# Kernel optimization log

Hardware: AMD Instinct MI355X
Metric: run time of the kernel (lower is better)

Reference implementation:

```python
import jax, jax.numpy as jnp
import numpy as np
from jax.ops import segment_sum

NUM_EMBEDDINGS = 512
EMBEDDING_DIM = 64
COMMITMENT_COST = 0.25
DECAY = 0.99
EPSILON = 1e-05


def setup_inputs() -> dict:
    key = jax.random.key(0)
    k1, k2, k3 = jax.random.split(key, 3)
    B, C, T = 32, EMBEDDING_DIM, 4096
    z = jax.random.normal(k1, (B, C, T), dtype=jnp.float32)
    embedding = jax.random.normal(k2, (NUM_EMBEDDINGS, EMBEDDING_DIM), dtype=jnp.float32)
    cluster_size = jnp.zeros((NUM_EMBEDDINGS,), dtype=jnp.float32)
    embed_avg = jax.random.normal(k3, (NUM_EMBEDDINGS, EMBEDDING_DIM), dtype=jnp.float32)
    return {"z": z, "embedding": embedding, "cluster_size": cluster_size, "embed_avg": embed_avg}


def reference(z, embedding, cluster_size, embed_avg):
    B, C, T = z.shape
    K = embedding.shape[0]
    # flatten: (B, C, T) -> (B*T, C), matching reshape(B,C,-1).permute(0,2,1).reshape(-1,C)
    z_flat = jnp.transpose(z, (0, 2, 1)).reshape(-1, C)  # [N, C]
    N = z_flat.shape[0]

    # squared-euclidean nearest-code search (argmin of cdist == argmin of sq dist)
    d2 = (jnp.sum(z_flat * z_flat, axis=1, keepdims=True)
          - 2.0 * (z_flat @ embedding.T)
          + jnp.sum(embedding * embedding, axis=1)[None, :])  # [N, K]
    indices = jnp.argmin(d2, axis=1)  # [N] int

    # quantize: gather instead of one-hot matmul (same math)
    quantized_flat = embedding[indices]  # [N, C]
    quantized = jnp.transpose(quantized_flat.reshape(B, T, C), (0, 2, 1))  # [B, C, T]

    # EMA codebook update (training branch)
    n = segment_sum(jnp.ones((N,), dtype=z.dtype), indices, num_segments=K)  # [K]
    new_cluster_size = cluster_size * DECAY + (1.0 - DECAY) * n
    embed_sum = segment_sum(z_flat, indices, num_segments=K)  # [K, C]
    new_embed_avg = embed_avg * DECAY + (1.0 - DECAY) * embed_sum
    n_tot = jnp.sum(new_cluster_size)
    cs_smoothed = (new_cluster_size + EPSILON) / (n_tot + K * EPSILON) * n_tot
    new_embedding = new_embed_avg / cs_smoothed[:, None]

    # commitment loss against detached quantized
    commitment_loss = jnp.mean((z - jax.lax.stop_gradient(quantized)) ** 2)
    vq_loss = COMMITMENT_COST * commitment_loss

    # straight-through estimator
    quantized_st = z + jax.lax.stop_gradient(quantized - z)

    # perplexity over code usage (zero-count codes contribute ~0, as in torch unique version)
    probs = n / N
    perplexity = jnp.exp(-jnp.sum(probs * jnp.log(probs + 1e-10)))

    return (quantized_st, indices, vq_loss, perplexity,
            new_embedding, new_cluster_size, new_embed_avg)
```

## Files before the change

kernel.cpp:

```cpp
#include <hip/hip_runtime.h>
#include <math.h>

#define KB_NUM 512
#define DIMC 64
#define BSZ 32
#define TLEN 4096
#define NTOK (BSZ * TLEN)
#define DECAY_F 0.99f
#define EPS_F 1e-5f
#define K2_SPAN 512

#define Q_OFF    ((size_t)0)
#define IDX_OFF  ((size_t)BSZ * DIMC * TLEN)
#define LOSS_OFF (IDX_OFF + (size_t)NTOK)
#define PLEX_OFF (LOSS_OFF + 1)
#define NEMB_OFF (PLEX_OFF + 1)
#define NCS_OFF  (NEMB_OFF + (size_t)KB_NUM * DIMC)
#define NEA_OFF  (NCS_OFF + (size_t)KB_NUM)

typedef _Float16 f16x8 __attribute__((ext_vector_type(8)));
typedef float    f32x4 __attribute__((ext_vector_type(4)));

__global__ __launch_bounds__(64) void vq_prep_e(
    const float* __restrict__ emb,
    _Float16* __restrict__ eh,
    _Float16* __restrict__ el,
    float* __restrict__ enorm)
{
    const int k = blockIdx.x;
    const int c = threadIdx.x;
    float v = emb[(size_t)k * DIMC + c];
    _Float16 h = (_Float16)v;
    eh[(size_t)k * DIMC + c] = h;
    el[(size_t)k * DIMC + c] = (_Float16)(v - (float)h);
    float s = v * v;
    #pragma unroll
    for (int off = 32; off > 0; off >>= 1)
        s += __shfl_down(s, off, 64);
    if (c == 0) enorm[k] = 0.5f * s;
}

__global__ __launch_bounds__(256, 2) void vq_main_kernel(
    const float* __restrict__ z,
    const float* __restrict__ emb,
    const _Float16* __restrict__ eh,
    const _Float16* __restrict__ el,
    const float* __restrict__ enorm,
    float* __restrict__ out,
    float* __restrict__ lossAcc)
{
    __shared__ float zs[256 * 65];

    const int tid = threadIdx.x;
    const int w   = tid >> 6;
    const int ln  = tid & 63;
    const int bk  = blockIdx.x;
    const int b   = bk >> 4;
    const int t0  = (bk & 15) << 8;

    const float* zg = z + (size_t)b * (DIMC * TLEN) + t0;

    #pragma unroll 8
    for (int c = 0; c < DIMC; ++c)
        zs[tid * 65 + c] = zg[(size_t)c * TLEN + tid];
    __syncthreads();

    f16x8 zhf[4][2], zlf[4][2];
    #pragma unroll
    for (int tt = 0; tt < 4; ++tt) {
        #pragma unroll
        for (int ks = 0; ks < 2; ++ks) {
            const float* zrow = &zs[(w * 64 + tt * 16 + (ln & 15)) * 65
                                    + ks * 32 + ((ln >> 4) << 3)];
            #pragma unroll
            for (int j = 0; j < 8; ++j) {
                float v = zrow[j];
                _Float16 h = (_Float16)v;
                zhf[tt][ks][j] = h;
                zlf[tt][ks][j] = (_Float16)(v - (float)h);
            }
        }
    }

    float bv[4] = {3.4e38f, 3.4e38f, 3.4e38f, 3.4e38f};
    int   bi[4] = {0, 0, 0, 0};

    #pragma unroll 1
    for (int chunk = 0; chunk < 8; ++chunk) {
        f32x4 acc[4][4];
        #pragma unroll
        for (int ct = 0; ct < 4; ++ct)
            #pragma unroll
            for (int tt = 0; tt < 4; ++tt)
                acc[ct][tt] = (f32x4){0.f, 0.f, 0.f, 0.f};

        #pragma unroll
        for (int ct = 0; ct < 4; ++ct) {
            const int crow = chunk * 64 + ct * 16 + (ln & 15);
            f16x8 ah[2], al[2];
            #pragma unroll
            for (int ks = 0; ks < 2; ++ks) {
                const size_t aoff = (size_t)crow * DIMC + ks * 32 + ((ln >> 4) << 3);
                ah[ks] = *(const f16x8*)(eh + aoff);
                al[ks] = *(const f16x8*)(el + aoff);
            }
            #pragma unroll
            for (int ks = 0; ks < 2; ++ks) {
                #pragma unroll
                for (int tt = 0; tt < 4; ++tt)
                    acc[ct][tt] = __builtin_amdgcn_mfma_f32_16x16x32_f16(
                        ah[ks], zhf[tt][ks], acc[ct][tt], 0, 0, 0);
                #pragma unroll
                for (int tt = 0; tt < 4; ++tt)
                    acc[ct][tt] = __builtin_amdgcn_mfma_f32_16x16x32_f16(
                        ah[ks], zlf[tt][ks], acc[ct][tt], 0, 0, 0);
                #pragma unroll
                for (int tt = 0; tt < 4; ++tt)
                    acc[ct][tt] = __builtin_amdgcn_mfma_f32_16x16x32_f16(
                        al[ks], zhf[tt][ks], acc[ct][tt], 0, 0, 0);
                #pragma unroll
                for (int tt = 0; tt < 4; ++tt)
                    acc[ct][tt] = __builtin_amdgcn_mfma_f32_16x16x32_f16(
                        al[ks], zlf[tt][ks], acc[ct][tt], 0, 0, 0);
            }
        }

        #pragma unroll
        for (int ct = 0; ct < 4; ++ct) {
            const int cb = chunk * 64 + ct * 16 + ((ln >> 4) << 2);
            float4 en = *(const float4*)(enorm + cb);
            const float e0 = en.x, e1 = en.y, e2 = en.z, e3 = en.w;
            #pragma unroll
            for (int tt = 0; tt < 4; ++tt) {
                float s0 = e0 - acc[ct][tt][0];
                float s1 = e1 - acc[ct][tt][1];
                float s2 = e2 - acc[ct][tt][2];
                float s3 = e3 - acc[ct][tt][3];
                if (s0 < bv[tt]) { bv[tt] = s0; bi[tt] = cb; }
                if (s1 < bv[tt]) { bv[tt] = s1; bi[tt] = cb + 1; }
                if (s2 < bv[tt]) { bv[tt] = s2; bi[tt] = cb + 2; }
                if (s3 < bv[tt]) { bv[tt] = s3; bi[tt] = cb + 3; }
            }
        }
    }

    #pragma unroll
    for (int mask = 16; mask <= 32; mask <<= 1) {
        #pragma unroll
        for (int tt = 0; tt < 4; ++tt) {
            float ov = __shfl_xor(bv[tt], mask, 64);
            int   oi = __shfl_xor(bi[tt], mask, 64);
            if (ov < bv[tt] || (ov == bv[tt] && oi < bi[tt])) {
                bv[tt] = ov; bi[tt] = oi;
            }
        }
    }

    const int g = ln >> 4;
    const int idxv = (g == 0) ? bi[0] : (g == 1) ? bi[1] : (g == 2) ? bi[2] : bi[3];
    const int tok = w * 64 + ln;

    out[IDX_OFF + (size_t)b * TLEN + t0 + tok] = (float)idxv;

    const float* er   = emb + (size_t)idxv * DIMC;
    const float* zrow = &zs[tok * 65];
    float* qo = out + (size_t)b * (DIMC * TLEN) + t0 + tok;

    float lsum = 0.f;
    #pragma unroll
    for (int c4 = 0; c4 < DIMC / 4; ++c4) {
        float4 ev = *(const float4*)(er + c4 * 4);
        float z0 = zrow[c4 * 4 + 0], z1 = zrow[c4 * 4 + 1];
        float z2 = zrow[c4 * 4 + 2], z3 = zrow[c4 * 4 + 3];
        float d0 = ev.x - z0, d1 = ev.y - z1, d2 = ev.z - z2, d3 = ev.w - z3;
        qo[(size_t)(c4 * 4 + 0) * TLEN] = z0 + d0;
        qo[(size_t)(c4 * 4 + 1) * TLEN] = z1 + d1;
        qo[(size_t)(c4 * 4 + 2) * TLEN] = z2 + d2;
        qo[(size_t)(c4 * 4 + 3) * TLEN] = z3 + d3;
        lsum = fmaf(d0, d0, lsum); lsum = fmaf(d1, d1, lsum);
        lsum = fmaf(d2, d2, lsum); lsum = fmaf(d3, d3, lsum);
    }

    #pragma unroll
    for (int off = 32; off > 0; off >>= 1)
        lsum += __shfl_down(lsum, off, 64);
    if (ln == 0) atomicAdd(lossAcc, lsum);
}

__global__ __launch_bounds__(256, 1) void vq_bin_kernel(
    const float* __restrict__ z,
    const float* __restrict__ out,
    float* __restrict__ cnt,
    float* __restrict__ esum,
    int R)
{
    __shared__ float acc[KB_NUM][DIMC + 1];
    __shared__ float scnt[KB_NUM];

    const int tid = threadIdx.x;
    for (int j = tid; j < KB_NUM * (DIMC + 1); j += 256) ((float*)acc)[j] = 0.f;
    for (int j = tid; j < KB_NUM; j += 256) scnt[j] = 0.f;
    __syncthreads();

    const int gt0 = blockIdx.x * K2_SPAN;
    #pragma unroll
    for (int it = 0; it < K2_SPAN / 256; ++it) {
        const int gt = gt0 + it * 256 + tid;
        const int b  = gt >> 12;
        const int t  = gt & (TLEN - 1);
        const int idx = (int)out[IDX_OFF + gt];
        atomicAdd(&scnt[idx], 1.0f);
        const float* zp = z + (size_t)b * (DIMC * TLEN) + t;
        #pragma unroll 4
        for (int c = 0; c < DIMC; ++c) {
            float zv = zp[(size_t)c * TLEN];
            atomicAdd(&acc[idx][c], zv);
        }
    }
    __syncthreads();

    const int r = (int)((unsigned)blockIdx.x % (unsigned)R);
    for (int j = tid; j < KB_NUM * DIMC; j += 256) {
        const int k = j >> 6, c = j & 63;
        float v = acc[k][c];
        if (v != 0.f) atomicAdd(esum + (size_t)r * (KB_NUM * DIMC) + j, v);
    }
    for (int j = tid; j < KB_NUM; j += 256) {
        float v = scnt[j];
        if (v != 0.f) atomicAdd(cnt + (size_t)r * KB_NUM + j, v);
    }
}

__global__ __launch_bounds__(512) void vq_stats_kernel(
    const float* __restrict__ cluster_size,
    const float* __restrict__ cnt,
    const float* __restrict__ lossAcc,
    float* __restrict__ out,
    float* __restrict__ ntotp,
    int R)
{
    const int k = threadIdx.x;

    float n = 0.f;
    #pragma unroll 4
    for (int r = 0; r < R; ++r) n += cnt[(size_t)r * KB_NUM + k];

    float ncs = cluster_size[k] * DECAY_F + (1.0f - DECAY_F) * n;
    out[NCS_OFF + k] = ncs;

    __shared__ float red[KB_NUM];

    red[k] = ncs;
    __syncthreads();
    for (int s = KB_NUM / 2; s > 0; s >>= 1) {
        if (k < s) red[k] += red[k + s];
        __syncthreads();
    }
    if (k == 0) ntotp[0] = red[0];
    __syncthreads();

    float p = n * (1.0f / (float)NTOK);
    red[k] = p * logf(p + 1e-10f);
    __syncthreads();
    for (int s = KB_NUM / 2; s > 0; s >>= 1) {
        if (k < s) red[k] += red[k + s];
        __syncthreads();
    }
    if (k == 0) {
        out[PLEX_OFF] = expf(-red[0]);
        out[LOSS_OFF] = 0.25f * lossAcc[0] * (1.0f / (float)(BSZ * DIMC * TLEN));
    }
}

__global__ __launch_bounds__(64) void vq_embed_kernel(
    const float* __restrict__ embed_avg,
    const float* __restrict__ esum,
    const float* __restrict__ ntotp,
    float* __restrict__ out,
    int R)
{
    const int k = blockIdx.x;
    const int c = threadIdx.x;

    float es = 0.f;
    #pragma unroll 4
    for (int r = 0; r < R; ++r)
        es += esum[((size_t)r * KB_NUM + k) * DIMC + c];

    float nea = embed_avg[(size_t)k * DIMC + c] * DECAY_F + (1.0f - DECAY_F) * es;
    out[NEA_OFF + (size_t)k * DIMC + c] = nea;

    float ncs  = out[NCS_OFF + k];
    float ntot = ntotp[0];
    float denom = (ncs + EPS_F) / (ntot + (float)KB_NUM * EPS_F) * ntot;
    out[NEMB_OFF + (size_t)k * DIMC + c] = nea / denom;
}

extern "C" void kernel_launch(void* const* d_in, const int* in_sizes, int n_in,
                              void* d_out, int out_size, void* d_ws, size_t ws_size,
                              hipStream_t stream)
{
    const float* z            = (const float*)d_in[0];
    const float* emb          = (const float*)d_in[1];
    const float* cluster_size = (const float*)d_in[2];
    const float* embed_avg    = (const float*)d_in[3];
    float* out = (float*)d_out;

    char* ws = (char*)d_ws;
    float*     lossAcc = (float*)ws;
    float*     ntotp   = (float*)(ws + 64);
    float*     enorm   = (float*)(ws + 256);
    _Float16*  eh      = (_Float16*)(ws + 4096);
    _Float16*  el      = (_Float16*)(ws + 4096 + 65536);
    const size_t CNT_OFF = 4096 + 131072;
    const size_t perR = (size_t)(KB_NUM + KB_NUM * DIMC) * sizeof(float);

    int R = 1;
    if (ws_size > CNT_OFF + perR)
        R = (int)((ws_size - CNT_OFF) / perR);
    if (R < 1) R = 1;
    if (R > 16) R = 16;

    float* cnt  = (float*)(ws + CNT_OFF);
    float* esum = cnt + (size_t)R * KB_NUM;

    hipMemsetAsync(ws, 0, 4096, stream);
    hipMemsetAsync(ws + CNT_OFF, 0, (size_t)R * perR, stream);

    vq_prep_e<<<dim3(KB_NUM), dim3(DIMC), 0, stream>>>(emb, eh, el, enorm);

    vq_main_kernel<<<dim3(NTOK / 256), dim3(256), 0, stream>>>(
        z, emb, eh, el, enorm, out, lossAcc);

    vq_bin_kernel<<<dim3(NTOK / K2_SPAN), dim3(256), 0, stream>>>(z, out, cnt, esum, R);

    vq_stats_kernel<<<dim3(1), dim3(512), 0, stream>>>(
        cluster_size, cnt, lossAcc, out, ntotp, R);

    vq_embed_kernel<<<dim3(KB_NUM), dim3(DIMC), 0, stream>>>(
        embed_avg, esum, ntotp, out, R);
}
```

Baseline: 153.7 us.

## Halve tokens per block in VQ search kernel and raise occupancy

```diff
diff --git a/kernel.cpp b/kernel.cpp
--- a/kernel.cpp
+++ b/kernel.cpp
@@ -9,6 +9,7 @@
 #define DECAY_F 0.99f
 #define EPS_F 1e-5f
 #define K2_SPAN 512
+#define MTOK 128
 
 #define Q_OFF    ((size_t)0)
 #define IDX_OFF  ((size_t)BSZ * DIMC * TLEN)
@@ -40,7 +41,7 @@
     if (c == 0) enorm[k] = 0.5f * s;
 }
 
-__global__ __launch_bounds__(256, 2) void vq_main_kernel(
+__global__ __launch_bounds__(256, 4) void vq_main_kernel(
     const float* __restrict__ z,
     const float* __restrict__ emb,
     const _Float16* __restrict__ eh,
@@ -49,28 +50,32 @@
     float* __restrict__ out,
     float* __restrict__ lossAcc)
 {
-    __shared__ float zs[256 * 65];
+    __shared__ float zs[MTOK * 65];
 
     const int tid = threadIdx.x;
     const int w   = tid >> 6;
     const int ln  = tid & 63;
     const int bk  = blockIdx.x;
-    const int b   = bk >> 4;
-    const int t0  = (bk & 15) << 8;
+    const int b   = bk >> 5;
+    const int t0  = (bk & 31) << 7;
 
     const float* zg = z + (size_t)b * (DIMC * TLEN) + t0;
 
-    #pragma unroll 8
-    for (int c = 0; c < DIMC; ++c)
-        zs[tid * 65 + c] = zg[(size_t)c * TLEN + tid];
-    __syncthreads();
-
-    f16x8 zhf[4][2], zlf[4][2];
-    #pragma unroll
-    for (int tt = 0; tt < 4; ++tt) {
+    {
+        const int tok   = tid & (MTOK - 1);
+        const int chalf = (tid >> 7) * 32;
+        #pragma unroll 8
+        for (int j = 0; j < 32; ++j)
+            zs[tok * 65 + chalf + j] = zg[(size_t)(chalf + j) * TLEN + tok];
+    }
+    __syncthreads();
+
+    f16x8 zhf[2][2], zlf[2][2];
+    #pragma unroll
+    for (int tt = 0; tt < 2; ++tt) {
         #pragma unroll
         for (int ks = 0; ks < 2; ++ks) {
-            const float* zrow = &zs[(w * 64 + tt * 16 + (ln & 15)) * 65
+            const float* zrow = &zs[(w * 32 + tt * 16 + (ln & 15)) * 65
                                     + ks * 32 + ((ln >> 4) << 3)];
             #pragma unroll
             for (int j = 0; j < 8; ++j) {
@@ -82,16 +87,16 @@
         }
     }
 
-    float bv[4] = {3.4e38f, 3.4e38f, 3.4e38f, 3.4e38f};
-    int   bi[4] = {0, 0, 0, 0};
+    float bv[2] = {3.4e38f, 3.4e38f};
+    int   bi[2] = {0, 0};
 
     #pragma unroll 1
     for (int chunk = 0; chunk < 8; ++chunk) {
-        f32x4 acc[4][4];
+        f32x4 acc[4][2];
         #pragma unroll
         for (int ct = 0; ct < 4; ++ct)
             #pragma unroll
-            for (int tt = 0; tt < 4; ++tt)
+            for (int tt = 0; tt < 2; ++tt)
                 acc[ct][tt] = (f32x4){0.f, 0.f, 0.f, 0.f};
 
         #pragma unroll
@@ -107,19 +112,19 @@
             #pragma unroll
             for (int ks = 0; ks < 2; ++ks) {
                 #pragma unroll
-                for (int tt = 0; tt < 4; ++tt)
+                for (int tt = 0; tt < 2; ++tt)
                     acc[ct][tt] = __builtin_amdgcn_mfma_f32_16x16x32_f16(
                         ah[ks], zhf[tt][ks], acc[ct][tt], 0, 0, 0);
                 #pragma unroll
-                for (int tt = 0; tt < 4; ++tt)
+                for (int tt = 0; tt < 2; ++tt)
                     acc[ct][tt] = __builtin_amdgcn_mfma_f32_16x16x32_f16(
                         ah[ks], zlf[tt][ks], acc[ct][tt], 0, 0, 0);
                 #pragma unroll
-                for (int tt = 0; tt < 4; ++tt)
+                for (int tt = 0; tt < 2; ++tt)
                     acc[ct][tt] = __builtin_amdgcn_mfma_f32_16x16x32_f16(
                         al[ks], zhf[tt][ks], acc[ct][tt], 0, 0, 0);
                 #pragma unroll
-                for (int tt = 0; tt < 4; ++tt)
+                for (int tt = 0; tt < 2; ++tt)
                     acc[ct][tt] = __builtin_amdgcn_mfma_f32_16x16x32_f16(
                         al[ks], zlf[tt][ks], acc[ct][tt], 0, 0, 0);
             }
@@ -131,7 +136,7 @@
             float4 en = *(const float4*)(enorm + cb);
             const float e0 = en.x, e1 = en.y, e2 = en.z, e3 = en.w;
             #pragma unroll
-            for (int tt = 0; tt < 4; ++tt) {
+            for (int tt = 0; tt < 2; ++tt) {
                 float s0 = e0 - acc[ct][tt][0];
                 float s1 = e1 - acc[ct][tt][1];
                 float s2 = e2 - acc[ct][tt][2];
@@ -147,7 +152,7 @@
     #pragma unroll
     for (int mask = 16; mask <= 32; mask <<= 1) {
         #pragma unroll
-        for (int tt = 0; tt < 4; ++tt) {
+        for (int tt = 0; tt < 2; ++tt) {
             float ov = __shfl_xor(bv[tt], mask, 64);
             int   oi = __shfl_xor(bi[tt], mask, 64);
             if (ov < bv[tt] || (ov == bv[tt] && oi < bi[tt])) {
@@ -156,19 +161,21 @@
         }
     }
 
-    const int g = ln >> 4;
-    const int idxv = (g == 0) ? bi[0] : (g == 1) ? bi[1] : (g == 2) ? bi[2] : bi[3];
-    const int tok = w * 64 + ln;
-
-    out[IDX_OFF + (size_t)b * TLEN + t0 + tok] = (float)idxv;
-
-    const float* er   = emb + (size_t)idxv * DIMC;
-    const float* zrow = &zs[tok * 65];
-    float* qo = out + (size_t)b * (DIMC * TLEN) + t0 + tok;
+    const int tte   = ln >> 5;
+    const int idxv  = tte ? bi[1] : bi[0];
+    const int tok   = w * 32 + tte * 16 + (ln & 15);
+    const int chalf = ((ln >> 4) & 1) * 32;
+
+    if (((ln >> 4) & 1) == 0)
+        out[IDX_OFF + (size_t)b * TLEN + t0 + tok] = (float)idxv;
+
+    const float* er   = emb + (size_t)idxv * DIMC + chalf;
+    const float* zrow = &zs[tok * 65 + chalf];
+    float* qo = out + (size_t)b * (DIMC * TLEN) + t0 + tok + (size_t)chalf * TLEN;
 
     float lsum = 0.f;
     #pragma unroll
-    for (int c4 = 0; c4 < DIMC / 4; ++c4) {
+    for (int c4 = 0; c4 < 8; ++c4) {
         float4 ev = *(const float4*)(er + c4 * 4);
         float z0 = zrow[c4 * 4 + 0], z1 = zrow[c4 * 4 + 1];
         float z2 = zrow[c4 * 4 + 2], z3 = zrow[c4 * 4 + 3];
@@ -324,12 +331,11 @@
     float* cnt  = (float*)(ws + CNT_OFF);
     float* esum = cnt + (size_t)R * KB_NUM;
 
-    hipMemsetAsync(ws, 0, 4096, stream);
-    hipMemsetAsync(ws + CNT_OFF, 0, (size_t)R * perR, stream);
+    hipMemsetAsync(ws, 0, CNT_OFF + (size_t)R * perR, stream);
 
     vq_prep_e<<<dim3(KB_NUM), dim3(DIMC), 0, stream>>>(emb, eh, el, enorm);
 
-    vq_main_kernel<<<dim3(NTOK / 256), dim3(256), 0, stream>>>(
+    vq_main_kernel<<<dim3(NTOK / MTOK), dim3(256), 0, stream>>>(
         z, emb, eh, el, enorm, out, lossAcc);
 
     vq_bin_kernel<<<dim3(NTOK / K2_SPAN), dim3(256), 0, stream>>>(z, out, cnt, esum, R);
```

After: 199.4 us. 1.3x slower.

## Pre-swizzle codebook into MFMA fragment layout and vectorize binning kernel

Applied to the files above, without the earlier changes.

```diff
diff --git a/kernel.cpp b/kernel.cpp
--- a/kernel.cpp
+++ b/kernel.cpp
@@ -8,7 +8,6 @@
 #define NTOK (BSZ * TLEN)
 #define DECAY_F 0.99f
 #define EPS_F 1e-5f
-#define K2_SPAN 512
 
 #define Q_OFF    ((size_t)0)
 #define IDX_OFF  ((size_t)BSZ * DIMC * TLEN)
@@ -23,16 +22,22 @@
 
 __global__ __launch_bounds__(64) void vq_prep_e(
     const float* __restrict__ emb,
-    _Float16* __restrict__ eh,
-    _Float16* __restrict__ el,
+    _Float16* __restrict__ efrag,
     float* __restrict__ enorm)
 {
     const int k = blockIdx.x;
     const int c = threadIdx.x;
     float v = emb[(size_t)k * DIMC + c];
     _Float16 h = (_Float16)v;
-    eh[(size_t)k * DIMC + c] = h;
-    el[(size_t)k * DIMC + c] = (_Float16)(v - (float)h);
+    _Float16 l = (_Float16)(v - (float)h);
+
+    const int kgrp = k >> 4, row = k & 15;
+    const int ks = c >> 5, seg = (c & 31) >> 3, j = c & 7;
+    const int lane = seg * 16 + row;
+    const size_t base = ((size_t)(kgrp * 2 + ks) * 2) * 512;
+    efrag[base + (size_t)lane * 8 + j]       = h;
+    efrag[base + 512 + (size_t)lane * 8 + j] = l;
+
     float s = v * v;
     #pragma unroll
     for (int off = 32; off > 0; off >>= 1)
@@ -43,8 +48,7 @@
 __global__ __launch_bounds__(256, 2) void vq_main_kernel(
     const float* __restrict__ z,
     const float* __restrict__ emb,
-    const _Float16* __restrict__ eh,
-    const _Float16* __restrict__ el,
+    const _Float16* __restrict__ efrag,
     const float* __restrict__ enorm,
     float* __restrict__ out,
     float* __restrict__ lossAcc)
@@ -96,14 +100,15 @@
 
         #pragma unroll
         for (int ct = 0; ct < 4; ++ct) {
-            const int crow = chunk * 64 + ct * 16 + (ln & 15);
+            const int kgrp = chunk * 4 + ct;
+            const _Float16* fb = efrag + ((size_t)kgrp * 4) * 512
+                                       + (size_t)ln * 8;
             f16x8 ah[2], al[2];
-            #pragma unroll
-            for (int ks = 0; ks < 2; ++ks) {
-                const size_t aoff = (size_t)crow * DIMC + ks * 32 + ((ln >> 4) << 3);
-                ah[ks] = *(const f16x8*)(eh + aoff);
-                al[ks] = *(const f16x8*)(el + aoff);
-            }
+            ah[0] = *(const f16x8*)(fb);
+            al[0] = *(const f16x8*)(fb + 512);
+            ah[1] = *(const f16x8*)(fb + 1024);
+            al[1] = *(const f16x8*)(fb + 1536);
+
             #pragma unroll
             for (int ks = 0; ks < 2; ++ks) {
                 #pragma unroll
@@ -202,20 +207,25 @@
     for (int j = tid; j < KB_NUM; j += 256) scnt[j] = 0.f;
     __syncthreads();
 
-    const int gt0 = blockIdx.x * K2_SPAN;
-    #pragma unroll
-    for (int it = 0; it < K2_SPAN / 256; ++it) {
-        const int gt = gt0 + it * 256 + tid;
-        const int b  = gt >> 12;
-        const int t  = gt & (TLEN - 1);
-        const int idx = (int)out[IDX_OFF + gt];
-        atomicAdd(&scnt[idx], 1.0f);
-        const float* zp = z + (size_t)b * (DIMC * TLEN) + t;
-        #pragma unroll 4
-        for (int c = 0; c < DIMC; ++c) {
-            float zv = zp[(size_t)c * TLEN];
-            atomicAdd(&acc[idx][c], zv);
-        }
+    const int gt = blockIdx.x * 1024 + tid * 4;
+    const int b  = gt >> 12;
+    const int t  = gt & (TLEN - 1);
+
+    float4 fi = *(const float4*)(out + IDX_OFF + gt);
+    const int i0 = (int)fi.x, i1 = (int)fi.y, i2 = (int)fi.z, i3 = (int)fi.w;
+    atomicAdd(&scnt[i0], 1.0f);
+    atomicAdd(&scnt[i1], 1.0f);
+    atomicAdd(&scnt[i2], 1.0f);
+    atomicAdd(&scnt[i3], 1.0f);
+
+    const float* zp = z + (size_t)b * (DIMC * TLEN) + t;
+    #pragma unroll 4
+    for (int c = 0; c < DIMC; ++c) {
+        float4 zv = *(const float4*)(zp + (size_t)c * TLEN);
+        atomicAdd(&acc[i0][c], zv.x);
+        atomicAdd(&acc[i1][c], zv.y);
+        atomicAdd(&acc[i2][c], zv.z);
+        atomicAdd(&acc[i3][c], zv.w);
     }
     __syncthreads();
 
@@ -310,8 +320,7 @@
     float*     lossAcc = (float*)ws;
     float*     ntotp   = (float*)(ws + 64);
     float*     enorm   = (float*)(ws + 256);
-    _Float16*  eh      = (_Float16*)(ws + 4096);
-    _Float16*  el      = (_Float16*)(ws + 4096 + 65536);
+    _Float16*  efrag   = (_Float16*)(ws + 4096);
     const size_t CNT_OFF = 4096 + 131072;
     const size_t perR = (size_t)(KB_NUM + KB_NUM * DIMC) * sizeof(float);
 
@@ -324,15 +333,14 @@
     float* cnt  = (float*)(ws + CNT_OFF);
     float* esum = cnt + (size_t)R * KB_NUM;
 
-    hipMemsetAsync(ws, 0, 4096, stream);
-    hipMemsetAsync(ws + CNT_OFF, 0, (size_t)R * perR, stream);
-
-    vq_prep_e<<<dim3(KB_NUM), dim3(DIMC), 0, stream>>>(emb, eh, el, enorm);
+    hipMemsetAsync(ws, 0, CNT_OFF + (size_t)R * perR, stream);
+
+    vq_prep_e<<<dim3(KB_NUM), dim3(DIMC), 0, stream>>>(emb, efrag, enorm);
 
     vq_main_kernel<<<dim3(NTOK / 256), dim3(256), 0, stream>>>(
-        z, emb, eh, el, enorm, out, lossAcc);
-
-    vq_bin_kernel<<<dim3(NTOK / K2_SPAN), dim3(256), 0, stream>>>(z, out, cnt, esum, R);
+        z, emb, efrag, enorm, out, lossAcc);
+
+    vq_bin_kernel<<<dim3(NTOK / 1024), dim3(256), 0, stream>>>(z, out, cnt, esum, R);
 
     vq_stats_kernel<<<dim3(1), dim3(512), 0, stream>>>(
         cluster_size, cnt, lossAcc, out, ntotp, R);
```

Measured after the change: 174.1 us. 13.3% more time.
